# Kernel tuning notes

Measured on AMD Instinct MI355X. Metric: run time of the kernel, lower is better.

The kernel has to match this reference:

```python
import jax, jax.numpy as jnp
import numpy as np

NEG_SLOPE = 0.2  # LeakyReLU slope used by GAT attention
EPS = 1e-16


def gat_conv(x, edge_index, W, a_src, a_dst, b):
    """One GATConv layer with 'mean' head aggregation.
    x: [N, Fin], edge_index: [2, E] (row 0 = src/j, row 1 = dst/i),
    W: [Fin, H*F], a_src/a_dst: [H, F], b: [F].
    Returns [N, F].
    """
    N = x.shape[0]
    H, F = a_src.shape
    h = (x @ W).reshape(N, H, F)                      # [N, H, F]
    src, dst = edge_index[0], edge_index[1]
    # per-node attention halves, gathered per edge
    as_ = jnp.einsum('nhf,hf->nh', h, a_src)          # [N, H]
    ad_ = jnp.einsum('nhf,hf->nh', h, a_dst)          # [N, H]
    e = jax.nn.leaky_relu(as_[src] + ad_[dst], NEG_SLOPE)  # [E, H]
    # segment softmax over incoming edges of each dst node
    m = jax.ops.segment_max(e, dst, num_segments=N)   # [N, H]
    ex = jnp.exp(e - m[dst])                          # [E, H]
    denom = jax.ops.segment_sum(ex, dst, num_segments=N)
    alpha = ex / (denom[dst] + EPS)                   # [E, H]
    # weighted scatter-aggregate of source features
    out = jax.ops.segment_sum(alpha[:, :, None] * h[src], dst, num_segments=N)  # [N, H, F]
    return out.mean(axis=1) + b                       # mean over heads


def setup_inputs() -> dict:
    key = jax.random.key(0)
    ks = jax.random.split(key, 10)
    N, E = 100000, 1000000
    in_dim, hid, out_dim, H = 128, 32, 16, 4
    x = jax.random.normal(ks[0], (N, in_dim), dtype=jnp.float32)
    edge_index = jax.random.randint(ks[1], (2, E), 0, N, dtype=jnp.int64)
    s1 = 1.0 / np.sqrt(in_dim)
    s2 = 1.0 / np.sqrt(hid)
    W1 = jax.random.uniform(ks[2], (in_dim, H * hid), jnp.float32, -s1, s1)
    a1_src = jax.random.uniform(ks[3], (H, hid), jnp.float32, -s2, s2)
    a1_dst = jax.random.uniform(ks[4], (H, hid), jnp.float32, -s2, s2)
    b1 = jnp.zeros((hid,), jnp.float32)
    s3 = 1.0 / np.sqrt(out_dim)
    W2 = jax.random.uniform(ks[5], (hid, H * out_dim), jnp.float32, -s2, s2)
    a2_src = jax.random.uniform(ks[6], (H, out_dim), jnp.float32, -s3, s3)
    a2_dst = jax.random.uniform(ks[7], (H, out_dim), jnp.float32, -s3, s3)
    b2 = jnp.zeros((out_dim,), jnp.float32)
    return {"x": x, "edge_index": edge_index,
            "W1": W1, "a1_src": a1_src, "a1_dst": a1_dst, "b1": b1,
            "W2": W2, "a2_src": a2_src, "a2_dst": a2_dst, "b2": b2}


def reference(x, edge_index, W1, a1_src, a1_dst, b1, W2, a2_src, a2_dst, b2):
    h = gat_conv(x, edge_index, W1, a1_src, a1_dst, b1)
    h = jax.nn.relu(h)
    # dropout is identity in eval mode
    out = gat_conv(h, edge_index, W2, a2_src, a2_dst, b2)
    return out
```

## Files before the change

kernel.cpp:

```cpp
#include <hip/hip_runtime.h>
#include <math.h>

#define NEG_SLOPE 0.2f
#define EPS_GAT 1e-16f
#define LOG2E 1.4426950408889634f
typedef unsigned int u32;
typedef unsigned short u16;
typedef __attribute__((ext_vector_type(8))) short short8;
typedef __attribute__((ext_vector_type(4))) float f32x4;

__device__ inline u16 f2bf(float x) {
    union { float f; u32 u; } v; v.f = x;
    u32 r = v.u + 0x7FFFu + ((v.u >> 16) & 1u);
    return (u16)(r >> 16);
}
__device__ inline float bf_lo(u32 u) {
    union { u32 i; float f; } v; v.i = u << 16; return v.f;
}
__device__ inline float bf_hi(u32 u) {
    union { u32 i; float f; } v; v.i = u & 0xFFFF0000u; return v.f;
}
__device__ inline float bf1(u16 s) {
    union { u32 i; float f; } v; v.i = ((u32)s) << 16; return v.f;
}
__device__ inline float fast_exp2(float x) {
#if __has_builtin(__builtin_amdgcn_exp2f)
    return __builtin_amdgcn_exp2f(x);
#else
    return exp2f(x);
#endif
}
__device__ inline float lrelu_exp2(float t) {
    return fast_exp2(fmaxf(t, NEG_SLOPE * t));
}


__global__ void w1_prep_kernel(const float* __restrict__ W1,
                               u16* __restrict__ w1t_hi, u16* __restrict__ w1t_lo) {
    int i = blockIdx.x * 256 + threadIdx.x;
    int k = i >> 7, n = i & 127;
    float w = W1[i];
    u16 hi = f2bf(w);
    u16 lo = f2bf(w - bf1(hi));
    w1t_hi[n * 128 + k] = hi;
    w1t_lo[n * 128 + k] = lo;
}


__global__ __launch_bounds__(256) void mega1_kernel(const float* __restrict__ X,
                                                    const u16* __restrict__ w1t_hi,
                                                    const u16* __restrict__ w1t_lo,
                                                    const float* __restrict__ a_src,
                                                    const float* __restrict__ a_dst,
                                                    u16* __restrict__ Hb,
                                                    float* __restrict__ as_,
                                                    float* __restrict__ ad_, int N,
                                                    const int* __restrict__ dst, int E,
                                                    int* __restrict__ counts, int* __restrict__ rank,
                                                    const float* __restrict__ W2,
                                                    const float* __restrict__ a2s,
                                                    const float* __restrict__ a2d,
                                                    float* __restrict__ w_as,
                                                    float* __restrict__ w_ad,
                                                    int gemmBlocks, int degBlocks) {
    __shared__ u16 xsh_hi[64][40];
    __shared__ u16 xsh_lo[64][40];
    __shared__ __align__(16) u16 wbuf[10240];
    __shared__ float ash[128], adsh[128];
    int b = blockIdx.x;
    int tid = threadIdx.x;

    if (b >= gemmBlocks) {
        if (b < gemmBlocks + degBlocks) {
            int e = (b - gemmBlocks) * 256 + tid;
            if (e < E) rank[e] = atomicAdd(&counts[dst[e]], 1);
        } else {
            if (tid < 128) {
                int h = tid >> 5, k = tid & 31;
                float s1 = 0.f, s2 = 0.f;
#pragma unroll
                for (int f = 0; f < 16; ++f) {
                    float w = W2[k * 64 + h * 16 + f];
                    s1 += w * a2s[h * 16 + f];
                    s2 += w * a2d[h * 16 + f];
                }
                w_as[h * 32 + k] = s1;
                w_ad[h * 32 + k] = s2;
            }
        }
        return;
    }

    u16* wsh_hi = wbuf;
    u16* wsh_lo = wbuf + 5120;
    int wave = tid >> 6, lane = tid & 63, quad = lane >> 4;
    int m0 = b * 64;

    if (tid < 128) { ash[tid] = a_src[tid]; adsh[tid] = a_dst[tid]; }

    f32x4 acc[4][2];
#pragma unroll
    for (int rt = 0; rt < 4; ++rt)
#pragma unroll
        for (int ct = 0; ct < 2; ++ct) acc[rt][ct] = (f32x4)(0.f);

    int xrow = tid >> 2, xkq = (tid & 3) * 8;

    for (int k0 = 0; k0 < 128; k0 += 32) {
        {
            int gr = m0 + xrow;
            float f[8];
            *(float4*)&f[0] = (gr < N) ? *(const float4*)(X + (size_t)gr * 128 + k0 + xkq)
                                       : make_float4(0.f, 0.f, 0.f, 0.f);
            *(float4*)&f[4] = (gr < N) ? *(const float4*)(X + (size_t)gr * 128 + k0 + xkq + 4)
                                       : make_float4(0.f, 0.f, 0.f, 0.f);
            u16 hi[8], lo[8];
#pragma unroll
            for (int i = 0; i < 8; ++i) {
                hi[i] = f2bf(f[i]);
                lo[i] = f2bf(f[i] - bf1(hi[i]));
            }
            *(uint4*)&xsh_hi[xrow][xkq] = *(uint4*)hi;
            *(uint4*)&xsh_lo[xrow][xkq] = *(uint4*)lo;
        }
        {
#pragma unroll
            for (int i = 0; i < 2; ++i) {
                int id = tid * 2 + i;
                int n = id >> 2, part = id & 3;
                *(uint4*)&wsh_hi[n * 40 + part * 8] =
                    ((const uint4*)(w1t_hi + n * 128 + k0))[part];
                *(uint4*)&wsh_lo[n * 40 + part * 8] =
                    ((const uint4*)(w1t_lo + n * 128 + k0))[part];
            }
        }
        __syncthreads();

        short8 bhi[2], blo[2];
#pragma unroll
        for (int ct = 0; ct < 2; ++ct) {
            int n = wave * 32 + ct * 16 + (lane & 15);
            bhi[ct] = *(const short8*)&wsh_hi[n * 40 + quad * 8];
            blo[ct] = *(const short8*)&wsh_lo[n * 40 + quad * 8];
        }
#pragma unroll
        for (int rt = 0; rt < 4; ++rt) {
            int m = rt * 16 + (lane & 15);
            short8 ahi = *(const short8*)&xsh_hi[m][quad * 8];
            short8 alo = *(const short8*)&xsh_lo[m][quad * 8];
#pragma unroll
            for (int ct = 0; ct < 2; ++ct) {
                acc[rt][ct] = __builtin_amdgcn_mfma_f32_16x16x32_bf16(ahi, bhi[ct], acc[rt][ct], 0, 0, 0);
                acc[rt][ct] = __builtin_amdgcn_mfma_f32_16x16x32_bf16(alo, bhi[ct], acc[rt][ct], 0, 0, 0);
                acc[rt][ct] = __builtin_amdgcn_mfma_f32_16x16x32_bf16(ahi, blo[ct], acc[rt][ct], 0, 0, 0);
            }
        }
        __syncthreads();
    }

    const int HS = 136;
#pragma unroll
    for (int rt = 0; rt < 4; ++rt)
#pragma unroll
        for (int ct = 0; ct < 2; ++ct) {
            int col = wave * 32 + ct * 16 + (lane & 15);
#pragma unroll
            for (int r = 0; r < 4; ++r) {
                int row = rt * 16 + quad * 4 + r;
                wbuf[row * HS + col] = f2bf(acc[rt][ct][r]);
            }
        }
    __syncthreads();

    {
        int row = tid >> 2, chunk = tid & 3;
        int gr = m0 + row;
        if (gr < N) {
            const uint4* sp = (const uint4*)&wbuf[row * HS + chunk * 32];
            uint4* dp = (uint4*)(Hb + (size_t)gr * 128 + chunk * 32);
#pragma unroll
            for (int k = 0; k < 4; ++k) dp[k] = sp[k];
        }
    }

    {
        int row = tid >> 2, h = tid & 3;
        int gr = m0 + row;
        if (gr < N) {
            const u32* hr = (const u32*)&wbuf[row * HS + h * 32];
            float s1 = 0.f, s2 = 0.f;
#pragma unroll
            for (int q = 0; q < 16; ++q) {
                u32 u = hr[q];
                float flo = bf_lo(u), fhi = bf_hi(u);
                s1 += flo * ash[h * 32 + 2 * q] + fhi * ash[h * 32 + 2 * q + 1];
                s2 += flo * adsh[h * 32 + 2 * q] + fhi * adsh[h * 32 + 2 * q + 1];
            }
            as_[(size_t)gr * 4 + h] = s1 * LOG2E;
            ad_[(size_t)gr * 4 + h] = s2 * LOG2E;
        }
    }
}

__global__ __launch_bounds__(1024) void scan_block_kernel(const int* __restrict__ counts, int N,
                                                          int* __restrict__ scanned, int* __restrict__ bsums) {
    __shared__ int tmp[1024];
    int i = blockIdx.x * 1024 + threadIdx.x;
    int v = (i < N) ? counts[i] : 0;
    tmp[threadIdx.x] = v;
    __syncthreads();
    for (int d = 1; d < 1024; d <<= 1) {
        int t = (threadIdx.x >= d) ? tmp[threadIdx.x - d] : 0;
        __syncthreads();
        tmp[threadIdx.x] += t;
        __syncthreads();
    }
    if (i < N) scanned[i] = tmp[threadIdx.x];
    if (threadIdx.x == 1023) bsums[blockIdx.x] = tmp[1023];
}

__global__ __launch_bounds__(256) void scan_partials_kernel(int* __restrict__ bsums, int nb) {
    __shared__ int tmp[256];
    int tid = threadIdx.x;
    int v = (tid < nb) ? bsums[tid] : 0;
    tmp[tid] = v;
    __syncthreads();
    for (int d = 1; d < 256; d <<= 1) {
        int t = (tid >= d) ? tmp[tid - d] : 0;
        __syncthreads();
        tmp[tid] += t;
        __syncthreads();
    }
    if (tid < nb) bsums[tid] = tmp[tid] - v;
}

__global__ void finalize_offsets_kernel(const int* __restrict__ scanned,
                                        const int* __restrict__ bsums_excl, int N,
                                        int* __restrict__ row_off) {
    int i = blockIdx.x * blockDim.x + threadIdx.x;
    if (i < N) {
        int incl = scanned[i] + bsums_excl[i >> 10];
        row_off[i + 1] = incl;
        if (i == 0) row_off[0] = 0;
    }
}

__global__ void fill_csr_kernel(const int* __restrict__ src, const int* __restrict__ dst, int E,
                                const int* __restrict__ row_off, const int* __restrict__ rank,
                                int* __restrict__ csr_src) {
    int e = blockIdx.x * blockDim.x + threadIdx.x;
    if (e < E) {
        int pos = row_off[dst[e]] + rank[e];
        csr_src[pos] = src[e];
    }
}


__global__ __launch_bounds__(256) void node_agg128_kernel(const u32* __restrict__ Hb,
                                                          const float* __restrict__ as_,
                                                          const float* __restrict__ ad_,
                                                          const int* __restrict__ row_off,
                                                          const int* __restrict__ csr_src,
                                                          const float* __restrict__ bias,
                                                          const float* __restrict__ w_as,
                                                          const float* __restrict__ w_ad,
                                                          u32* __restrict__ O1,
                                                          float* __restrict__ as2,
                                                          float* __restrict__ ad2, int N) {
    int lane = threadIdx.x & 63;
    int node = __builtin_amdgcn_readfirstlane(blockIdx.x * 4 + (threadIdx.x >> 6));
    if (node >= N) return;
    int start = __builtin_amdgcn_readfirstlane(row_off[node]);
    int end   = __builtin_amdgcn_readfirstlane(row_off[node + 1]);
    int deg = end - start;
    int h = lane >> 4;
    float adh = ad_[node * 4 + h];

    int clamp = (deg > 0) ? deg - 1 : 0;
    int vidx = csr_src[start + min(lane, clamp)];
    int m = min(deg, 64);

    float2 acc = make_float2(0.f, 0.f);
    float den = 0.f;
    int j = 0;
    for (; j + 4 <= m; j += 4) {
        int s0 = __builtin_amdgcn_readlane(vidx, j);
        int s1 = __builtin_amdgcn_readlane(vidx, j + 1);
        int s2 = __builtin_amdgcn_readlane(vidx, j + 2);
        int s3 = __builtin_amdgcn_readlane(vidx, j + 3);
        float a0 = as_[s0 * 4 + h], a1 = as_[s1 * 4 + h];
        float a2 = as_[s2 * 4 + h], a3 = as_[s3 * 4 + h];
        u32 u0 = Hb[s0 * 64 + lane];
        u32 u1 = Hb[s1 * 64 + lane];
        u32 u2 = Hb[s2 * 64 + lane];
        u32 u3 = Hb[s3 * 64 + lane];
        float e0 = lrelu_exp2(a0 + adh), e1 = lrelu_exp2(a1 + adh);
        float e2 = lrelu_exp2(a2 + adh), e3 = lrelu_exp2(a3 + adh);
        acc.x = fmaf(e0, bf_lo(u0), acc.x); acc.y = fmaf(e0, bf_hi(u0), acc.y); den += e0;
        acc.x = fmaf(e1, bf_lo(u1), acc.x); acc.y = fmaf(e1, bf_hi(u1), acc.y); den += e1;
        acc.x = fmaf(e2, bf_lo(u2), acc.x); acc.y = fmaf(e2, bf_hi(u2), acc.y); den += e2;
        acc.x = fmaf(e3, bf_lo(u3), acc.x); acc.y = fmaf(e3, bf_hi(u3), acc.y); den += e3;
    }
    for (; j < m; ++j) {
        int s = __builtin_amdgcn_readlane(vidx, j);
        float e = lrelu_exp2(as_[s * 4 + h] + adh);
        u32 u = Hb[s * 64 + lane];
        acc.x = fmaf(e, bf_lo(u), acc.x); acc.y = fmaf(e, bf_hi(u), acc.y); den += e;
    }
    for (int jj = start + 64; jj < end; ++jj) {
        int s = __builtin_amdgcn_readfirstlane(csr_src[jj]);
        float e = lrelu_exp2(as_[s * 4 + h] + adh);
        u32 u = Hb[s * 64 + lane];
        acc.x = fmaf(e, bf_lo(u), acc.x); acc.y = fmaf(e, bf_hi(u), acc.y); den += e;
    }
    float inv = 1.f / (den + EPS_GAT);
    float px = acc.x * inv, py = acc.y * inv;
    px += __shfl_xor(px, 16); py += __shfl_xor(py, 16);
    px += __shfl_xor(px, 32); py += __shfl_xor(py, 32);

    int f2 = (lane & 15) * 2;
    float2 bv = *(const float2*)&bias[f2];
    float ox = fmaxf(px * 0.25f + bv.x, 0.f);
    float oy = fmaxf(py * 0.25f + bv.y, 0.f);
    if (lane < 16)
        O1[node * 16 + lane] = (u32)f2bf(ox) | ((u32)f2bf(oy) << 16);

    int h2 = lane >> 4;
    float2 wa = *(const float2*)&w_as[h2 * 32 + f2];
    float2 wd = *(const float2*)&w_ad[h2 * 32 + f2];
    float ta = ox * wa.x + oy * wa.y;
    float td = ox * wd.x + oy * wd.y;
    ta += __shfl_xor(ta, 1); td += __shfl_xor(td, 1);
    ta += __shfl_xor(ta, 2); td += __shfl_xor(td, 2);
    ta += __shfl_xor(ta, 4); td += __shfl_xor(td, 4);
    ta += __shfl_xor(ta, 8); td += __shfl_xor(td, 8);
    if ((lane & 15) == 0) {
        as2[node * 4 + h2] = ta * LOG2E;
        ad2[node * 4 + h2] = td * LOG2E;
    }
}


__global__ __launch_bounds__(256) void node_agg32_fused_kernel(const u32* __restrict__ O1,
                                                               const float* __restrict__ as_,
                                                               const float* __restrict__ ad_,
                                                               const int* __restrict__ row_off,
                                                               const int* __restrict__ csr_src,
                                                               const float* __restrict__ W2,
                                                               const float* __restrict__ b2,
                                                               float* __restrict__ Out, int N) {
    __shared__ float w2sh[2048];
    __shared__ float aggsh[4][136];
    int tid = threadIdx.x;
    {
        float4 v = ((const float4*)W2)[tid];
        *(float4*)&w2sh[tid * 4] = v;
        float4 v2 = ((const float4*)W2)[tid + 256];
        *(float4*)&w2sh[(tid + 256) * 4] = v2;
    }

    int lane = tid & 63;
    int nb = tid >> 6;
    int node = __builtin_amdgcn_readfirstlane(blockIdx.x * 4 + nb);
    bool active = node < N;
    int h = lane >> 4, f = lane & 15;
    if (active) {
        int start = __builtin_amdgcn_readfirstlane(row_off[node]);
        int end   = __builtin_amdgcn_readfirstlane(row_off[node + 1]);
        int deg = end - start;
        float adh = ad_[node * 4 + h];

        int clamp = (deg > 0) ? deg - 1 : 0;
        int vidx = csr_src[start + min(lane, clamp)];
        int m = min(deg, 64);

        float2 acc = make_float2(0.f, 0.f);
        float den = 0.f;
        int j = 0;
        for (; j + 4 <= m; j += 4) {
            int s0 = __builtin_amdgcn_readlane(vidx, j);
            int s1 = __builtin_amdgcn_readlane(vidx, j + 1);
            int s2 = __builtin_amdgcn_readlane(vidx, j + 2);
            int s3 = __builtin_amdgcn_readlane(vidx, j + 3);
            float a0 = as_[s0 * 4 + h], a1 = as_[s1 * 4 + h];
            float a2 = as_[s2 * 4 + h], a3 = as_[s3 * 4 + h];
            u32 u0 = O1[s0 * 16 + f];
            u32 u1 = O1[s1 * 16 + f];
            u32 u2 = O1[s2 * 16 + f];
            u32 u3 = O1[s3 * 16 + f];
            float e0 = lrelu_exp2(a0 + adh), e1 = lrelu_exp2(a1 + adh);
            float e2 = lrelu_exp2(a2 + adh), e3 = lrelu_exp2(a3 + adh);
            acc.x = fmaf(e0, bf_lo(u0), acc.x); acc.y = fmaf(e0, bf_hi(u0), acc.y); den += e0;
            acc.x = fmaf(e1, bf_lo(u1), acc.x); acc.y = fmaf(e1, bf_hi(u1), acc.y); den += e1;
            acc.x = fmaf(e2, bf_lo(u2), acc.x); acc.y = fmaf(e2, bf_hi(u2), acc.y); den += e2;
            acc.x = fmaf(e3, bf_lo(u3), acc.x); acc.y = fmaf(e3, bf_hi(u3), acc.y); den += e3;
        }
        for (; j < m; ++j) {
            int s = __builtin_amdgcn_readlane(vidx, j);
            float e = lrelu_exp2(as_[s * 4 + h] + adh);
            u32 u = O1[s * 16 + f];
            acc.x = fmaf(e, bf_lo(u), acc.x); acc.y = fmaf(e, bf_hi(u), acc.y); den += e;
        }
        for (int jj = start + 64; jj < end; ++jj) {
            int s = __builtin_amdgcn_readfirstlane(csr_src[jj]);
            float e = lrelu_exp2(as_[s * 4 + h] + adh);
            u32 u = O1[s * 16 + f];
            acc.x = fmaf(e, bf_lo(u), acc.x); acc.y = fmaf(e, bf_hi(u), acc.y); den += e;
        }
        float inv = 1.f / (den + EPS_GAT);
        aggsh[nb][h * 34 + f * 2]     = acc.x * inv;
        aggsh[nb][h * 34 + f * 2 + 1] = acc.y * inv;
    }
    __syncthreads();

    if (active) {
        int q = h, o = f;
        float s = 0.f;
#pragma unroll
        for (int k = 0; k < 32; ++k)
            s += aggsh[nb][q * 34 + k] * w2sh[k * 64 + q * 16 + o];
        s += __shfl_xor(s, 16);
        s += __shfl_xor(s, 32);
        if (lane < 16)
            Out[(size_t)node * 16 + o] = s * 0.25f + b2[o];
    }
}


extern "C" void kernel_launch(void* const* d_in, const int* in_sizes, int n_in,
                              void* d_out, int out_size, void* d_ws, size_t ws_size,
                              hipStream_t stream) {
    const float* x      = (const float*)d_in[0];
    const int*   eidx   = (const int*)d_in[1];
    const float* W1     = (const float*)d_in[2];
    const float* a1_src = (const float*)d_in[3];
    const float* a1_dst = (const float*)d_in[4];
    const float* b1     = (const float*)d_in[5];
    const float* W2     = (const float*)d_in[6];
    const float* a2_src = (const float*)d_in[7];
    const float* a2_dst = (const float*)d_in[8];
    const float* b2     = (const float*)d_in[9];
    float* out = (float*)d_out;

    const int N = in_sizes[0] / 128;
    const int E = in_sizes[1] / 2;
    const int* src = eidx;
    const int* dst = eidx + E;

    char* base = (char*)d_ws;
    size_t off = 0;
    auto carve = [&](size_t bytes) -> char* {
        off = (off + 255) & ~(size_t)255;
        char* p = base + off;
        off += bytes;
        return p;
    };
    int* counts   = (int*)carve((size_t)N * 4);
    int* scanned  = (int*)carve((size_t)N * 4);
    int* bsums    = (int*)carve(256 * 4);
    int* row_off  = (int*)carve((size_t)(N + 1) * 4);
    int* rank     = (int*)carve((size_t)E * 4);
    int* csr_src  = (int*)carve((size_t)E * 4);
    u16* w1t_hi   = (u16*)carve(128 * 128 * 2);
    u16* w1t_lo   = (u16*)carve(128 * 128 * 2);
    u16* h1b      = (u16*)carve((size_t)N * 128 * 2);
    u32* out1b    = (u32*)carve((size_t)N * 16 * 4);
    float* as1  = (float*)carve((size_t)N * 4 * 4);
    float* ad1  = (float*)carve((size_t)N * 4 * 4);
    float* as2  = (float*)carve((size_t)N * 4 * 4);
    float* ad2  = (float*)carve((size_t)N * 4 * 4);
    float* w_as = (float*)carve(4 * 32 * 4);
    float* w_ad = (float*)carve(4 * 32 * 4);
    (void)ws_size; (void)n_in; (void)out_size;

    hipMemsetAsync(counts, 0, (size_t)N * 4, stream);
    w1_prep_kernel<<<64, 256, 0, stream>>>(W1, w1t_hi, w1t_lo);

    int gemmBlocks = (N + 63) / 64;
    int degBlocks = (E + 255) / 256;
    mega1_kernel<<<gemmBlocks + degBlocks + 1, 256, 0, stream>>>(
        x, w1t_hi, w1t_lo, a1_src, a1_dst, h1b, as1, ad1, N,
        dst, E, counts, rank,
        W2, a2_src, a2_dst, w_as, w_ad,
        gemmBlocks, degBlocks);

    int nb = (N + 1023) / 1024;
    scan_block_kernel<<<nb, 1024, 0, stream>>>(counts, N, scanned, bsums);
    scan_partials_kernel<<<1, 256, 0, stream>>>(bsums, nb);
    finalize_offsets_kernel<<<(N + 255) / 256, 256, 0, stream>>>(scanned, bsums, N, row_off);
    fill_csr_kernel<<<(E + 255) / 256, 256, 0, stream>>>(src, dst, E, row_off, rank, csr_src);

    node_agg128_kernel<<<(N + 3) / 4, 256, 0, stream>>>((const u32*)h1b, as1, ad1,
                                                        row_off, csr_src, b1, w_as, w_ad,
                                                        out1b, as2, ad2, N);

    node_agg32_fused_kernel<<<(N + 3) / 4, 256, 0, stream>>>(out1b, as2, ad2, row_off,
                                                             csr_src, W2, b2, out, N);
}
```

Before: 286.6 us.

## Split CSR fill by destination half and overlap second half with aggregation

The memset of the degree counts is folded into the W1 prep kernel as extra blocks, removing one separate operation. The CSR fill is split into two passes by destination node range. The second pass runs in the same launch as layer-1 aggregation over the first half of the nodes, and a final launch aggregates the remaining nodes. The aim is to hide the scatter-fill latency behind aggregation work. The cost is that each fill pass reads all edges twice and adds one more kernel launch.

Result: no change. 290.9 us (+1.5%).

```diff
diff --git a/kernel.cpp b/kernel.cpp
--- a/kernel.cpp
+++ b/kernel.cpp
@@ -36,14 +36,21 @@
 
 
 __global__ void w1_prep_kernel(const float* __restrict__ W1,
-                               u16* __restrict__ w1t_hi, u16* __restrict__ w1t_lo) {
-    int i = blockIdx.x * 256 + threadIdx.x;
-    int k = i >> 7, n = i & 127;
-    float w = W1[i];
-    u16 hi = f2bf(w);
-    u16 lo = f2bf(w - bf1(hi));
-    w1t_hi[n * 128 + k] = hi;
-    w1t_lo[n * 128 + k] = lo;
+                               u16* __restrict__ w1t_hi, u16* __restrict__ w1t_lo,
+                               int* __restrict__ counts, int N) {
+    int b = blockIdx.x;
+    if (b < 64) {
+        int i = b * 256 + threadIdx.x;
+        int k = i >> 7, n = i & 127;
+        float w = W1[i];
+        u16 hi = f2bf(w);
+        u16 lo = f2bf(w - bf1(hi));
+        w1t_hi[n * 128 + k] = hi;
+        w1t_lo[n * 128 + k] = lo;
+    } else {
+        int i = (b - 64) * 256 + threadIdx.x;
+        if (i < N) counts[i] = 0;
+    }
 }
 
 
@@ -245,31 +252,42 @@
     }
 }
 
+
+__device__ __forceinline__ void fill_body(const int* __restrict__ src,
+                                          const int* __restrict__ dst, int E,
+                                          const int* __restrict__ row_off,
+                                          const int* __restrict__ rank,
+                                          int* __restrict__ csr_src,
+                                          int e, int dstLo, int dstHi) {
+    if (e < E) {
+        int d = dst[e];
+        if (d >= dstLo && d < dstHi) {
+            int pos = row_off[d] + rank[e];
+            csr_src[pos] = src[e];
+        }
+    }
+}
+
 __global__ void fill_csr_kernel(const int* __restrict__ src, const int* __restrict__ dst, int E,
                                 const int* __restrict__ row_off, const int* __restrict__ rank,
-                                int* __restrict__ csr_src) {
+                                int* __restrict__ csr_src, int dstLo, int dstHi) {
     int e = blockIdx.x * blockDim.x + threadIdx.x;
-    if (e < E) {
-        int pos = row_off[dst[e]] + rank[e];
-        csr_src[pos] = src[e];
-    }
-}
-
-
-__global__ __launch_bounds__(256) void node_agg128_kernel(const u32* __restrict__ Hb,
-                                                          const float* __restrict__ as_,
-                                                          const float* __restrict__ ad_,
-                                                          const int* __restrict__ row_off,
-                                                          const int* __restrict__ csr_src,
-                                                          const float* __restrict__ bias,
-                                                          const float* __restrict__ w_as,
-                                                          const float* __restrict__ w_ad,
-                                                          u32* __restrict__ O1,
-                                                          float* __restrict__ as2,
-                                                          float* __restrict__ ad2, int N) {
-    int lane = threadIdx.x & 63;
-    int node = __builtin_amdgcn_readfirstlane(blockIdx.x * 4 + (threadIdx.x >> 6));
-    if (node >= N) return;
+    fill_body(src, dst, E, row_off, rank, csr_src, e, dstLo, dstHi);
+}
+
+
+__device__ __forceinline__ void agg128_body(const u32* __restrict__ Hb,
+                                            const float* __restrict__ as_,
+                                            const float* __restrict__ ad_,
+                                            const int* __restrict__ row_off,
+                                            const int* __restrict__ csr_src,
+                                            const float* __restrict__ bias,
+                                            const float* __restrict__ w_as,
+                                            const float* __restrict__ w_ad,
+                                            u32* __restrict__ O1,
+                                            float* __restrict__ as2,
+                                            float* __restrict__ ad2,
+                                            int node, int lane) {
     int start = __builtin_amdgcn_readfirstlane(row_off[node]);
     int end   = __builtin_amdgcn_readfirstlane(row_off[node + 1]);
     int deg = end - start;
@@ -337,6 +355,54 @@
     if ((lane & 15) == 0) {
         as2[node * 4 + h2] = ta * LOG2E;
         ad2[node * 4 + h2] = td * LOG2E;
+    }
+}
+
+__global__ __launch_bounds__(256) void node_agg128_kernel(const u32* __restrict__ Hb,
+                                                          const float* __restrict__ as_,
+                                                          const float* __restrict__ ad_,
+                                                          const int* __restrict__ row_off,
+                                                          const int* __restrict__ csr_src,
+                                                          const float* __restrict__ bias,
+                                                          const float* __restrict__ w_as,
+                                                          const float* __restrict__ w_ad,
+                                                          u32* __restrict__ O1,
+                                                          float* __restrict__ as2,
+                                                          float* __restrict__ ad2,
+                                                          int node0, int nodeEnd) {
+    int lane = threadIdx.x & 63;
+    int node = __builtin_amdgcn_readfirstlane(node0 + blockIdx.x * 4 + (threadIdx.x >> 6));
+    if (node >= nodeEnd) return;
+    agg128_body(Hb, as_, ad_, row_off, csr_src, bias, w_as, w_ad, O1, as2, ad2, node, lane);
+}
+
+
+__global__ __launch_bounds__(256) void agg128_fill_kernel(const u32* __restrict__ Hb,
+                                                          const float* __restrict__ as_,
+                                                          const float* __restrict__ ad_,
+                                                          const int* __restrict__ row_off,
+                                                          const int* __restrict__ csr_src_ro,
+                                                          const float* __restrict__ bias,
+                                                          const float* __restrict__ w_as,
+                                                          const float* __restrict__ w_ad,
+                                                          u32* __restrict__ O1,
+                                                          float* __restrict__ as2,
+                                                          float* __restrict__ ad2,
+                                                          int nodeEnd, int aggBlocks,
+                                                          const int* __restrict__ src,
+                                                          const int* __restrict__ dst, int E,
+                                                          const int* __restrict__ rank,
+                                                          int* __restrict__ csr_src_w,
+                                                          int dstLo, int dstHi) {
+    int b = blockIdx.x;
+    if (b < aggBlocks) {
+        int lane = threadIdx.x & 63;
+        int node = __builtin_amdgcn_readfirstlane(b * 4 + (threadIdx.x >> 6));
+        if (node >= nodeEnd) return;
+        agg128_body(Hb, as_, ad_, row_off, csr_src_ro, bias, w_as, w_ad, O1, as2, ad2, node, lane);
+    } else {
+        int e = (b - aggBlocks) * 256 + threadIdx.x;
+        fill_body(src, dst, E, row_off, rank, csr_src_w, e, dstLo, dstHi);
     }
 }
 
@@ -473,8 +539,8 @@
     float* w_ad = (float*)carve(4 * 32 * 4);
     (void)ws_size; (void)n_in; (void)out_size;
 
-    hipMemsetAsync(counts, 0, (size_t)N * 4, stream);
-    w1_prep_kernel<<<64, 256, 0, stream>>>(W1, w1t_hi, w1t_lo);
+    int zeroBlocks = (N + 255) / 256;
+    w1_prep_kernel<<<64 + zeroBlocks, 256, 0, stream>>>(W1, w1t_hi, w1t_lo, counts, N);
 
     int gemmBlocks = (N + 63) / 64;
     int degBlocks = (E + 255) / 256;
@@ -488,11 +554,22 @@
     scan_block_kernel<<<nb, 1024, 0, stream>>>(counts, N, scanned, bsums);
     scan_partials_kernel<<<1, 256, 0, stream>>>(bsums, nb);
     finalize_offsets_kernel<<<(N + 255) / 256, 256, 0, stream>>>(scanned, bsums, N, row_off);
-    fill_csr_kernel<<<(E + 255) / 256, 256, 0, stream>>>(src, dst, E, row_off, rank, csr_src);
-
-    node_agg128_kernel<<<(N + 3) / 4, 256, 0, stream>>>((const u32*)h1b, as1, ad1,
-                                                        row_off, csr_src, b1, w_as, w_ad,
-                                                        out1b, as2, ad2, N);
+
+    int NH = ((N / 2) + 3) & ~3;
+    if (NH > N) NH = N;
+    fill_csr_kernel<<<degBlocks, 256, 0, stream>>>(src, dst, E, row_off, rank, csr_src, 0, NH);
+
+    int aggB1 = (NH + 3) / 4;
+    agg128_fill_kernel<<<aggB1 + degBlocks, 256, 0, stream>>>(
+        (const u32*)h1b, as1, ad1, row_off, csr_src, b1, w_as, w_ad,
+        out1b, as2, ad2, NH, aggB1,
+        src, dst, E, rank, csr_src, NH, N);
+
+    int aggB2 = (N - NH + 3) / 4;
+    if (aggB2 > 0)
+        node_agg128_kernel<<<aggB2, 256, 0, stream>>>((const u32*)h1b, as1, ad1,
+                                                      row_off, csr_src, b1, w_as, w_ad,
+                                                      out1b, as2, ad2, NH, N);
 
     node_agg32_fused_kernel<<<(N + 3) / 4, 256, 0, stream>>>(out1b, as2, ad2, row_off,
                                                              csr_src, W2, b2, out, N);
```
